# Performance work log

Hardware: AMD Instinct MI355X
Metric: run time of the kernel (lower is better)

Reference implementation:

```python
import jax, jax.numpy as jnp
import numpy as np

B, N_MM, N_V, N_A = 2, 256, 64, 128
DIM, HEADS, ATTN_RATIO, MLP_RATIO = 1024, 16, 0.25, 4.0
INNER = int(DIM * ATTN_RATIO)          # 256
HID = int(DIM * MLP_RATIO)             # 4096
SCALE = (DIM // HEADS) ** -0.5         # faithful to source: uses dim//num_heads
EPS = 1e-5


def setup_inputs() -> dict:
    key = jax.random.key(0)
    ks = jax.random.split(key, 16)
    s = 0.02
    return {
        "xmm": jax.random.normal(ks[0], (B, N_MM, DIM), jnp.float32),
        "xv": jax.random.normal(ks[1], (B, N_V, DIM), jnp.float32),
        "xa": jax.random.normal(ks[2], (B, N_A, DIM), jnp.float32),
        "ln_mm_w": jnp.ones((DIM,), jnp.float32),
        "ln_mm_b": jnp.zeros((DIM,), jnp.float32),
        "ln_v_w": jnp.ones((DIM,), jnp.float32),
        "ln_v_b": jnp.zeros((DIM,), jnp.float32),
        "ln_a_w": jnp.ones((DIM,), jnp.float32),
        "ln_a_b": jnp.zeros((DIM,), jnp.float32),
        "Wq": jax.random.normal(ks[3], (DIM, INNER), jnp.float32) * s,
        "Wkv": jax.random.normal(ks[4], (2 * DIM, 2 * INNER), jnp.float32) * s,
        "Wproj": jax.random.normal(ks[5], (INNER, DIM), jnp.float32) * s,
        "bproj": jnp.zeros((DIM,), jnp.float32),
        "ln_mlp_w": jnp.ones((DIM,), jnp.float32),
        "ln_mlp_b": jnp.zeros((DIM,), jnp.float32),
        "W1": jax.random.normal(ks[6], (DIM, HID), jnp.float32) * s,
        "b1": jnp.zeros((HID,), jnp.float32),
        "W2": jax.random.normal(ks[7], (HID, DIM), jnp.float32) * s,
        "b2": jnp.zeros((DIM,), jnp.float32),
    }


def _ln(x, w, b):
    m = x.mean(-1, keepdims=True)
    v = ((x - m) ** 2).mean(-1, keepdims=True)
    return (x - m) / jnp.sqrt(v + EPS) * w + b


def reference(xmm, xv, xa, ln_mm_w, ln_mm_b, ln_v_w, ln_v_b, ln_a_w, ln_a_b,
              Wq, Wkv, Wproj, bproj, ln_mlp_w, ln_mlp_b, W1, b1, W2, b2):
    hd = INNER // HEADS
    src_mm = _ln(xmm, ln_mm_w, ln_mm_b)
    src_v = _ln(xv, ln_v_w, ln_v_b)
    src_a = _ln(xa, ln_a_w, ln_a_b)

    # kv(x_va) where x_va = cat([xv broadcast over N_a, xa broadcast over N_v], -1).
    # Equivalent to projecting each stream separately and broadcast-adding:
    kv_v = src_v @ Wkv[:DIM]            # [B, N_v, 2*INNER]
    kv_a = src_a @ Wkv[DIM:]            # [B, N_a, 2*INNER]
    kv = kv_v[:, :, None, :] + kv_a[:, None, :, :]          # [B, N_v, N_a, 2*INNER]
    kv = kv.reshape(B, N_V * N_A, 2, HEADS, hd)
    k = kv[:, :, 0].transpose(0, 2, 1, 3)                   # [B, H, N_va, hd]
    v = kv[:, :, 1].transpose(0, 2, 1, 3)

    q = (src_mm @ Wq).reshape(B, N_MM, HEADS, hd).transpose(0, 2, 1, 3)

    attn = jnp.einsum('bhqd,bhkd->bhqk', q, k) * SCALE
    attn = jax.nn.softmax(attn, axis=-1)
    out = jnp.einsum('bhqk,bhkd->bhqd', attn, v)
    out = out.transpose(0, 2, 1, 3).reshape(B, N_MM, INNER)
    out = out @ Wproj + bproj

    xmm = xmm + out
    h = _ln(xmm, ln_mlp_w, ln_mlp_b)
    h = jax.nn.gelu(h @ W1 + b1, approximate=False) @ W2 + b2
    return xmm + h
```

## Files before the change

### kernel.cpp

```cpp
#include <hip/hip_runtime.h>
#include <hip/hip_bf16.h>
#include <math.h>


typedef unsigned short ushort_t;
typedef __attribute__((ext_vector_type(8))) __bf16 bf16x8;
typedef __attribute__((ext_vector_type(4))) float f32x4;

#define DEVFN static __device__ __forceinline__

DEVFN float bf2f(ushort_t u) {
    return __uint_as_float(((unsigned int)u) << 16);
}
DEVFN ushort_t f2bf(float f) {
    unsigned int x = __float_as_uint(f);
    unsigned int r = x + 0x7FFFu + ((x >> 16) & 1u);
    return (ushort_t)(r >> 16);
}
DEVFN void unpack8(uint4 dv, float* dst) {
    unsigned int ws[4] = {dv.x, dv.y, dv.z, dv.w};
#pragma unroll
    for (int i = 0; i < 4; i++) {
        dst[2 * i] = __uint_as_float(ws[i] << 16);
        dst[2 * i + 1] = __uint_as_float(ws[i] & 0xFFFF0000u);
    }
}

DEVFN void ln_body(const float* __restrict__ x, const float* __restrict__ w,
                   const float* __restrict__ b, ushort_t* __restrict__ out,
                   int row) {
    const float4* xr4 = (const float4*)(x + (size_t)row * 1024);
    ushort_t* orow = out + (size_t)row * 1024;
    int tid = threadIdx.x;
    float4 v4 = xr4[tid];
    float s = v4.x + v4.y + v4.z + v4.w;
    float ss = v4.x * v4.x + v4.y * v4.y + v4.z * v4.z + v4.w * v4.w;
#pragma unroll
    for (int off = 32; off > 0; off >>= 1) {
        s += __shfl_down(s, off);
        ss += __shfl_down(ss, off);
    }
    __shared__ float red[8];
    if ((tid & 63) == 0) {
        red[tid >> 6] = s;
        red[4 + (tid >> 6)] = ss;
    }
    __syncthreads();
    s = red[0] + red[1] + red[2] + red[3];
    ss = red[4] + red[5] + red[6] + red[7];
    float mean = s * (1.f / 1024.f);
    float var = ss * (1.f / 1024.f) - mean * mean;
    float rstd = rsqrtf(var + 1e-5f);
    const float4 w4 = ((const float4*)w)[tid];
    const float4 b4 = ((const float4*)b)[tid];
    union { ushort_t u[4]; uint2 v; } pk;
    pk.u[0] = f2bf((v4.x - mean) * rstd * w4.x + b4.x);
    pk.u[1] = f2bf((v4.y - mean) * rstd * w4.y + b4.y);
    pk.u[2] = f2bf((v4.z - mean) * rstd * w4.z + b4.z);
    pk.u[3] = f2bf((v4.w - mean) * rstd * w4.w + b4.w);
    *(uint2*)(&orow[tid * 4]) = pk.v;
}

__global__ __launch_bounds__(256) void ln_kernel(
    const float* __restrict__ x, const float* __restrict__ w,
    const float* __restrict__ b, ushort_t* __restrict__ out) {
    ln_body(x, w, b, out, blockIdx.x);
}

struct LNSeg {
    const float* x; const float* w; const float* b; ushort_t* out; int start;
};
struct TDesc { const float* in; ushort_t* out; int R, C, nx, start; };

__global__ __launch_bounds__(256) void prep_kernel(LNSeg l0, LNSeg l1,
                                                   LNSeg l2, TDesc d0,
                                                   TDesc d1, TDesc d2,
                                                   TDesc d3, TDesc d4) {
    int id = blockIdx.x;
    if (id < 896) {
        LNSeg s = (id >= l2.start) ? l2 : ((id >= l1.start) ? l1 : l0);
        ln_body(s.x, s.w, s.b, s.out, id - s.start);
        return;
    }
    id -= 896;
    TDesc d = (id >= d4.start) ? d4
            : (id >= d3.start) ? d3
            : (id >= d2.start) ? d2
            : (id >= d1.start) ? d1 : d0;
    int t = id - d.start;
    int bx = (t % d.nx) * 32;
    int by = (t / d.nx) * 32;
    __shared__ ushort_t tile[32][33];
    int tx = threadIdx.x & 31;
    int ty = threadIdx.x >> 5;
    for (int i = ty; i < 32; i += 8)
        tile[i][tx] = f2bf(d.in[(size_t)(by + i) * d.C + bx + tx]);
    __syncthreads();
    for (int i = ty; i < 32; i += 8)
        d.out[(size_t)(bx + i) * d.R + by + tx] = tile[tx][i];
}

template <int EPI, typename OutT>
DEVFN void gemm64_core(const ushort_t* __restrict__ A, int lda,
                       const ushort_t* __restrict__ B, int ldb,
                       OutT* __restrict__ C, int ldc,
                       const float* __restrict__ bias,
                       const float* __restrict__ resid, int K, int m0, int n0,
                       ushort_t* As, ushort_t* Bs) {
    constexpr int LS = 40;
    int tid = threadIdx.x;
    int wave = tid >> 6, lane = tid & 63;
    int wm = wave >> 1, wn = wave & 1;
    int quad = lane >> 4, l16 = lane & 15;

    f32x4 acc[2][2];
#pragma unroll
    for (int i = 0; i < 2; i++)
#pragma unroll
        for (int j = 0; j < 2; j++) acc[i][j] = (f32x4){0.f, 0.f, 0.f, 0.f};

    int r = tid >> 2, c = tid & 3;
    const ushort_t* Ap = A + (size_t)(m0 + r) * lda + c * 8;
    const ushort_t* Bp = B + (size_t)(n0 + r) * ldb + c * 8;
    uint4 ra = *(const uint4*)Ap;
    uint4 rb = *(const uint4*)Bp;

    for (int k0 = 0; k0 < K; k0 += 32) {
        *(uint4*)(&As[r * LS + c * 8]) = ra;
        *(uint4*)(&Bs[r * LS + c * 8]) = rb;
        __syncthreads();
        if (k0 + 32 < K) {
            ra = *(const uint4*)(Ap + k0 + 32);
            rb = *(const uint4*)(Bp + k0 + 32);
        }
        bf16x8 af[2], bfr[2];
#pragma unroll
        for (int i = 0; i < 2; i++)
            af[i] = *(const bf16x8*)(&As[(wm * 32 + i * 16 + l16) * LS + quad * 8]);
#pragma unroll
        for (int j = 0; j < 2; j++)
            bfr[j] = *(const bf16x8*)(&Bs[(wn * 32 + j * 16 + l16) * LS + quad * 8]);
#pragma unroll
        for (int i = 0; i < 2; i++)
#pragma unroll
            for (int j = 0; j < 2; j++)
                acc[i][j] = __builtin_amdgcn_mfma_f32_16x16x32_bf16(
                    af[i], bfr[j], acc[i][j], 0, 0, 0);
        __syncthreads();
    }

#pragma unroll
    for (int i = 0; i < 2; i++)
#pragma unroll
        for (int j = 0; j < 2; j++) {
            int col = n0 + wn * 32 + j * 16 + l16;
            int rbase = m0 + wm * 32 + i * 16 + quad * 4;
            float bv = (EPI == 2 || EPI == 3) ? bias[col] : 0.f;
#pragma unroll
            for (int rr = 0; rr < 4; rr++) {
                int row = rbase + rr;
                float vv = acc[i][j][rr] + bv;
                if (EPI == 2) vv = 0.5f * vv * (1.f + erff(vv * 0.70710678118654752f));
                if (EPI == 3) vv += resid[(size_t)row * ldc + col];
                if constexpr (sizeof(OutT) == 2)
                    C[(size_t)row * ldc + col] = (OutT)f2bf(vv);
                else
                    C[(size_t)row * ldc + col] = vv;
            }
        }
}

template <int EPI, typename OutT>
__global__ __launch_bounds__(256) void gemm64(
    const ushort_t* __restrict__ A, int lda, const ushort_t* __restrict__ Bt,
    int ldb, OutT* __restrict__ C, int ldc, const float* __restrict__ bias,
    const float* __restrict__ resid, int Kper, int sliceStride) {
    __shared__ ushort_t As[64 * 40];
    __shared__ ushort_t Bs[64 * 40];
    int z = blockIdx.z;
    gemm64_core<EPI, OutT>(A + (size_t)z * Kper, lda, Bt + (size_t)z * Kper,
                           ldb, C + (size_t)z * sliceStride, ldc, bias, resid,
                           Kper, blockIdx.y * 64, blockIdx.x * 64, As, Bs);
}

struct GSeg {
    const ushort_t* A; const ushort_t* B; ushort_t* C;
    int lda, ldb, ldc, nx, start;
};
__global__ __launch_bounds__(256) void gemm64_multi(GSeg s0, GSeg s1, GSeg s2,
                                                    int K) {
    __shared__ ushort_t As[64 * 40];
    __shared__ ushort_t Bs[64 * 40];
    int id = blockIdx.x;
    GSeg s = (id >= s2.start) ? s2 : ((id >= s1.start) ? s1 : s0);
    int t = id - s.start;
    int n0 = (t % s.nx) * 64;
    int m0 = (t / s.nx) * 64;
    gemm64_core<0, ushort_t>(s.A, s.lda, s.B, s.ldb, s.C, s.ldc, nullptr,
                             nullptr, K, m0, n0, As, Bs);
}

__global__ __launch_bounds__(256) void reduce_mlp2(
    const float* __restrict__ P, const float* __restrict__ y,
    const float* __restrict__ b2, float* __restrict__ out) {
    int i = blockIdx.x * 256 + threadIdx.x;
    const float4* p = (const float4*)P;
    float4 a = p[i], b = p[i + 131072], cc = p[i + 2 * 131072],
           d = p[i + 3 * 131072];
    float4 yy = ((const float4*)y)[i];
    float4 bb = ((const float4*)b2)[i & 255];
    float4 o;
    o.x = a.x + b.x + cc.x + d.x + yy.x + bb.x;
    o.y = a.y + b.y + cc.y + d.y + yy.y + bb.y;
    o.z = a.z + b.z + cc.z + d.z + yy.z + bb.z;
    o.w = a.w + b.w + cc.w + d.w + yy.w + bb.w;
    ((float4*)out)[i] = o;
}

__global__ __launch_bounds__(256) void attn_kernel(
    const ushort_t* __restrict__ q, const ushort_t* __restrict__ kvv,
    const ushort_t* __restrict__ kva, ushort_t* __restrict__ out) {
    int bh = blockIdx.x;
    int b = bh >> 4, h = bh & 15;
    int tid = threadIdx.x;

    __shared__ float Kv[64][16], Vv[64][16], Ka[128][16], Va[128][16];

    {
        int row = tid >> 2, seg = (tid >> 1) & 1, half = tid & 1;
        const ushort_t* src =
            kvv + (size_t)(b * 64 + row) * 512 + seg * 256 + h * 16 + half * 8;
        float* dst = (seg ? Vv[row] : Kv[row]) + half * 8;
        unpack8(*(const uint4*)src, dst);
    }
#pragma unroll
    for (int t2 = 0; t2 < 2; t2++) {
        int t = tid + t2 * 256;
        int row = t >> 2, seg = (t >> 1) & 1, half = t & 1;
        const ushort_t* src =
            kva + (size_t)(b * 128 + row) * 512 + seg * 256 + h * 16 + half * 8;
        float* dst = (seg ? Va[row] : Ka[row]) + half * 8;
        unpack8(*(const uint4*)src, dst);
    }
    __syncthreads();

    int qlocal = tid >> 2;
    int dg = tid & 3;
    int qrow = blockIdx.y * 64 + qlocal;
    const ushort_t* qp = q + (size_t)(b * 256 + qrow) * 256 + h * 16 + dg * 4;
    uint2 qu = *(const uint2*)qp;
    float4 qv;
    qv.x = __uint_as_float(qu.x << 16) * 0.125f;
    qv.y = __uint_as_float(qu.x & 0xFFFF0000u) * 0.125f;
    qv.z = __uint_as_float(qu.y << 16) * 0.125f;
    qv.w = __uint_as_float(qu.y & 0xFFFF0000u) * 0.125f;

    const float4* Kv4 = (const float4*)Kv;
    const float4* Vv4 = (const float4*)Vv;
    const float4* Ka4 = (const float4*)Ka;
    const float4* Va4 = (const float4*)Va;

    float4 ov = {0.f, 0.f, 0.f, 0.f};
    float den = 0.f;
#pragma unroll 8
    for (int i = 0; i < 64; i++) {
        float4 kk = Kv4[i * 4 + dg];
        float part = qv.x * kk.x + qv.y * kk.y + qv.z * kk.z + qv.w * kk.w;
        part += __shfl_xor(part, 1);
        part += __shfl_xor(part, 2);
        float p = __expf(part);
        den += p;
        float4 vv = Vv4[i * 4 + dg];
        ov.x += p * vv.x; ov.y += p * vv.y; ov.z += p * vv.z; ov.w += p * vv.w;
    }
    float4 oa = {0.f, 0.f, 0.f, 0.f};
    float dena = 0.f;
#pragma unroll 8
    for (int i = 0; i < 128; i++) {
        float4 kk = Ka4[i * 4 + dg];
        float part = qv.x * kk.x + qv.y * kk.y + qv.z * kk.z + qv.w * kk.w;
        part += __shfl_xor(part, 1);
        part += __shfl_xor(part, 2);
        float p = __expf(part);
        dena += p;
        float4 vv = Va4[i * 4 + dg];
        oa.x += p * vv.x; oa.y += p * vv.y; oa.z += p * vv.z; oa.w += p * vv.w;
    }

    float rv = 1.f / den, ra = 1.f / dena;
    union { ushort_t u[4]; uint2 v; } pk;
    pk.u[0] = f2bf(ov.x * rv + oa.x * ra);
    pk.u[1] = f2bf(ov.y * rv + oa.y * ra);
    pk.u[2] = f2bf(ov.z * rv + oa.z * ra);
    pk.u[3] = f2bf(ov.w * rv + oa.w * ra);
    *(uint2*)(out + (size_t)(b * 256 + qrow) * 256 + h * 16 + dg * 4) = pk.v;
}

extern "C" void kernel_launch(void* const* d_in, const int* in_sizes, int n_in,
                              void* d_out, int out_size, void* d_ws,
                              size_t ws_size, hipStream_t stream) {
    const float* xmm = (const float*)d_in[0];
    const float* xv = (const float*)d_in[1];
    const float* xa = (const float*)d_in[2];
    const float* ln_mm_w = (const float*)d_in[3];
    const float* ln_mm_b = (const float*)d_in[4];
    const float* ln_v_w = (const float*)d_in[5];
    const float* ln_v_b = (const float*)d_in[6];
    const float* ln_a_w = (const float*)d_in[7];
    const float* ln_a_b = (const float*)d_in[8];
    const float* Wq = (const float*)d_in[9];
    const float* Wkv = (const float*)d_in[10];
    const float* Wproj = (const float*)d_in[11];
    const float* bproj = (const float*)d_in[12];
    const float* ln_mlp_w = (const float*)d_in[13];
    const float* ln_mlp_b = (const float*)d_in[14];
    const float* W1 = (const float*)d_in[15];
    const float* b1 = (const float*)d_in[16];
    const float* W2 = (const float*)d_in[17];
    const float* b2 = (const float*)d_in[18];
    float* outp = (float*)d_out;

    char* w = (char*)d_ws;
    ushort_t* xmmN = (ushort_t*)w;    w += 512 * 1024 * 2;
    ushort_t* xvN = (ushort_t*)w;     w += 128 * 1024 * 2;
    ushort_t* xaN = (ushort_t*)w;     w += 256 * 1024 * 2;
    ushort_t* Wqt = (ushort_t*)w;     w += 256 * 1024 * 2;
    ushort_t* Wkvt = (ushort_t*)w;    w += 512 * 2048 * 2;
    ushort_t* Wprojt = (ushort_t*)w;  w += 1024 * 256 * 2;
    ushort_t* W1t = (ushort_t*)w;     w += 4096 * 1024 * 2;
    ushort_t* W2t = (ushort_t*)w;     w += 1024 * 4096 * 2;
    ushort_t* qout = (ushort_t*)w;    w += 512 * 256 * 2;
    ushort_t* kvvb = (ushort_t*)w;    w += 128 * 512 * 2;
    ushort_t* kvab = (ushort_t*)w;    w += 256 * 512 * 2;
    ushort_t* attnout = (ushort_t*)w; w += 512 * 256 * 2;
    float* y = (float*)w;             w += 512 * 1024 * 4;
    ushort_t* h0 = (ushort_t*)w;      w += 512 * 1024 * 2;
    ushort_t* g = (ushort_t*)w;       w += 512 * 4096 * 2;
    float* P = (float*)w;             w += 4 * 512 * 1024 * 4;

    LNSeg L0{xmm, ln_mm_w, ln_mm_b, xmmN, 0};
    LNSeg L1{xv, ln_v_w, ln_v_b, xvN, 512};
    LNSeg L2{xa, ln_a_w, ln_a_b, xaN, 640};
    TDesc T0{Wq, Wqt, 1024, 256, 8, 0};
    TDesc T1{Wkv, Wkvt, 2048, 512, 16, 256};
    TDesc T2{Wproj, Wprojt, 256, 1024, 32, 1280};
    TDesc T3{W1, W1t, 1024, 4096, 128, 1536};
    TDesc T4{W2, W2t, 4096, 1024, 32, 5632};
    prep_kernel<<<896 + 9728, 256, 0, stream>>>(L0, L1, L2, T0, T1, T2, T3, T4);

    GSeg G0{xmmN, Wqt, qout, 1024, 1024, 256, 4, 0};
    GSeg G1{xvN, Wkvt, kvvb, 1024, 2048, 512, 8, 32};
    GSeg G2{xaN, Wkvt + 1024, kvab, 1024, 2048, 512, 8, 48};
    gemm64_multi<<<80, 256, 0, stream>>>(G0, G1, G2, 1024);

    attn_kernel<<<dim3(32, 4), 256, 0, stream>>>(qout, kvvb, kvab, attnout);

    gemm64<3, float><<<dim3(16, 8, 1), 256, 0, stream>>>(
        attnout, 256, Wprojt, 256, y, 1024, bproj, xmm, 256, 0);

    ln_kernel<<<512, 256, 0, stream>>>(y, ln_mlp_w, ln_mlp_b, h0);

    gemm64<2, ushort_t><<<dim3(64, 8, 1), 256, 0, stream>>>(
        h0, 1024, W1t, 1024, g, 4096, b1, nullptr, 1024, 0);

    gemm64<4, float><<<dim3(16, 8, 4), 256, 0, stream>>>(
        g, 4096, W2t, 4096, P, 1024, nullptr, nullptr, 1024, 512 * 1024);

    reduce_mlp2<<<512, 256, 0, stream>>>(P, y, b2, outp);

    (void)in_sizes; (void)n_in; (void)out_size; (void)ws_size;
}
```

Measured before the change: 201.9 us.

## Fuse all stages into one cooperative persistent kernel with grid syncs

Replaces the eight separate kernel launches with a single cooperative mega-kernel of 512 persistent blocks. Each stage loops over its work items and is separated from the next by grid.sync(). The aim is to remove per-launch overhead and the inter-kernel gaps. The weight-transpose tiles are also changed to use float4 loads and packed uint2 stores. The cost is that every stage boundary becomes a grid-wide barrier, and small stages (80 or 128 items) leave most of the 512 blocks idle.

```diff
diff --git a/kernel.cpp b/kernel.cpp
--- a/kernel.cpp
+++ b/kernel.cpp
@@ -1,6 +1,9 @@
 #include <hip/hip_runtime.h>
 #include <hip/hip_bf16.h>
+#include <hip/hip_cooperative_groups.h>
 #include <math.h>
+
+namespace cg = cooperative_groups;
 
 
 typedef unsigned short ushort_t;
@@ -26,9 +29,23 @@
     }
 }
 
+struct MegaParams {
+    const float *xmm, *xv, *xa;
+    const float *ln_mm_w, *ln_mm_b, *ln_v_w, *ln_v_b, *ln_a_w, *ln_a_b;
+    const float *Wq, *Wkv, *Wproj, *bproj, *ln_mlp_w, *ln_mlp_b;
+    const float *W1, *b1, *W2, *b2;
+    float* outp;
+    ushort_t *xmmN, *xvN, *xaN;
+    ushort_t *Wqt, *Wkvt, *Wprojt, *W1t, *W2t;
+    ushort_t *qout, *kvvb, *kvab, *attnout;
+    float* y;
+    ushort_t *h0, *g;
+    float* P;
+};
+
 DEVFN void ln_body(const float* __restrict__ x, const float* __restrict__ w,
                    const float* __restrict__ b, ushort_t* __restrict__ out,
-                   int row) {
+                   int row, float* red) {
     const float4* xr4 = (const float4*)(x + (size_t)row * 1024);
     ushort_t* orow = out + (size_t)row * 1024;
     int tid = threadIdx.x;
@@ -40,7 +57,6 @@
         s += __shfl_down(s, off);
         ss += __shfl_down(ss, off);
     }
-    __shared__ float red[8];
     if ((tid & 63) == 0) {
         red[tid >> 6] = s;
         red[4 + (tid >> 6)] = ss;
@@ -61,52 +77,13 @@
     *(uint2*)(&orow[tid * 4]) = pk.v;
 }
 
-__global__ __launch_bounds__(256) void ln_kernel(
-    const float* __restrict__ x, const float* __restrict__ w,
-    const float* __restrict__ b, ushort_t* __restrict__ out) {
-    ln_body(x, w, b, out, blockIdx.x);
-}
-
-struct LNSeg {
-    const float* x; const float* w; const float* b; ushort_t* out; int start;
-};
-struct TDesc { const float* in; ushort_t* out; int R, C, nx, start; };
-
-__global__ __launch_bounds__(256) void prep_kernel(LNSeg l0, LNSeg l1,
-                                                   LNSeg l2, TDesc d0,
-                                                   TDesc d1, TDesc d2,
-                                                   TDesc d3, TDesc d4) {
-    int id = blockIdx.x;
-    if (id < 896) {
-        LNSeg s = (id >= l2.start) ? l2 : ((id >= l1.start) ? l1 : l0);
-        ln_body(s.x, s.w, s.b, s.out, id - s.start);
-        return;
-    }
-    id -= 896;
-    TDesc d = (id >= d4.start) ? d4
-            : (id >= d3.start) ? d3
-            : (id >= d2.start) ? d2
-            : (id >= d1.start) ? d1 : d0;
-    int t = id - d.start;
-    int bx = (t % d.nx) * 32;
-    int by = (t / d.nx) * 32;
-    __shared__ ushort_t tile[32][33];
-    int tx = threadIdx.x & 31;
-    int ty = threadIdx.x >> 5;
-    for (int i = ty; i < 32; i += 8)
-        tile[i][tx] = f2bf(d.in[(size_t)(by + i) * d.C + bx + tx]);
-    __syncthreads();
-    for (int i = ty; i < 32; i += 8)
-        d.out[(size_t)(bx + i) * d.R + by + tx] = tile[tx][i];
-}
-
 template <int EPI, typename OutT>
-DEVFN void gemm64_core(const ushort_t* __restrict__ A, int lda,
-                       const ushort_t* __restrict__ B, int ldb,
-                       OutT* __restrict__ C, int ldc,
-                       const float* __restrict__ bias,
-                       const float* __restrict__ resid, int K, int m0, int n0,
-                       ushort_t* As, ushort_t* Bs) {
+DEVFN void gemm_item(const ushort_t* __restrict__ A, int lda,
+                     const ushort_t* __restrict__ B, int ldb,
+                     OutT* __restrict__ C, int ldc,
+                     const float* __restrict__ bias,
+                     const float* __restrict__ resid, int K, int m0, int n0,
+                     ushort_t* As, ushort_t* Bs) {
     constexpr int LS = 40;
     int tid = threadIdx.x;
     int wave = tid >> 6, lane = tid & 63;
@@ -170,203 +147,256 @@
         }
 }
 
-template <int EPI, typename OutT>
-__global__ __launch_bounds__(256) void gemm64(
-    const ushort_t* __restrict__ A, int lda, const ushort_t* __restrict__ Bt,
-    int ldb, OutT* __restrict__ C, int ldc, const float* __restrict__ bias,
-    const float* __restrict__ resid, int Kper, int sliceStride) {
-    __shared__ ushort_t As[64 * 40];
-    __shared__ ushort_t Bs[64 * 40];
-    int z = blockIdx.z;
-    gemm64_core<EPI, OutT>(A + (size_t)z * Kper, lda, Bt + (size_t)z * Kper,
-                           ldb, C + (size_t)z * sliceStride, ldc, bias, resid,
-                           Kper, blockIdx.y * 64, blockIdx.x * 64, As, Bs);
-}
-
-struct GSeg {
-    const ushort_t* A; const ushort_t* B; ushort_t* C;
-    int lda, ldb, ldc, nx, start;
-};
-__global__ __launch_bounds__(256) void gemm64_multi(GSeg s0, GSeg s1, GSeg s2,
-                                                    int K) {
-    __shared__ ushort_t As[64 * 40];
-    __shared__ ushort_t Bs[64 * 40];
-    int id = blockIdx.x;
-    GSeg s = (id >= s2.start) ? s2 : ((id >= s1.start) ? s1 : s0);
-    int t = id - s.start;
-    int n0 = (t % s.nx) * 64;
-    int m0 = (t / s.nx) * 64;
-    gemm64_core<0, ushort_t>(s.A, s.lda, s.B, s.ldb, s.C, s.ldc, nullptr,
-                             nullptr, K, m0, n0, As, Bs);
-}
-
-__global__ __launch_bounds__(256) void reduce_mlp2(
-    const float* __restrict__ P, const float* __restrict__ y,
-    const float* __restrict__ b2, float* __restrict__ out) {
-    int i = blockIdx.x * 256 + threadIdx.x;
-    const float4* p = (const float4*)P;
-    float4 a = p[i], b = p[i + 131072], cc = p[i + 2 * 131072],
-           d = p[i + 3 * 131072];
-    float4 yy = ((const float4*)y)[i];
-    float4 bb = ((const float4*)b2)[i & 255];
-    float4 o;
-    o.x = a.x + b.x + cc.x + d.x + yy.x + bb.x;
-    o.y = a.y + b.y + cc.y + d.y + yy.y + bb.y;
-    o.z = a.z + b.z + cc.z + d.z + yy.z + bb.z;
-    o.w = a.w + b.w + cc.w + d.w + yy.w + bb.w;
-    ((float4*)out)[i] = o;
-}
-
-__global__ __launch_bounds__(256) void attn_kernel(
-    const ushort_t* __restrict__ q, const ushort_t* __restrict__ kvv,
-    const ushort_t* __restrict__ kva, ushort_t* __restrict__ out) {
-    int bh = blockIdx.x;
-    int b = bh >> 4, h = bh & 15;
+__global__ __launch_bounds__(256, 2) void mega_kernel(MegaParams p) {
+    cg::grid_group grid = cg::this_grid();
+    __shared__ alignas(16) unsigned char smem[24576];
     int tid = threadIdx.x;
-
-    __shared__ float Kv[64][16], Vv[64][16], Ka[128][16], Va[128][16];
-
-    {
-        int row = tid >> 2, seg = (tid >> 1) & 1, half = tid & 1;
-        const ushort_t* src =
-            kvv + (size_t)(b * 64 + row) * 512 + seg * 256 + h * 16 + half * 8;
-        float* dst = (seg ? Vv[row] : Kv[row]) + half * 8;
-        unpack8(*(const uint4*)src, dst);
-    }
-#pragma unroll
-    for (int t2 = 0; t2 < 2; t2++) {
-        int t = tid + t2 * 256;
-        int row = t >> 2, seg = (t >> 1) & 1, half = t & 1;
-        const ushort_t* src =
-            kva + (size_t)(b * 128 + row) * 512 + seg * 256 + h * 16 + half * 8;
-        float* dst = (seg ? Va[row] : Ka[row]) + half * 8;
-        unpack8(*(const uint4*)src, dst);
-    }
-    __syncthreads();
-
-    int qlocal = tid >> 2;
-    int dg = tid & 3;
-    int qrow = blockIdx.y * 64 + qlocal;
-    const ushort_t* qp = q + (size_t)(b * 256 + qrow) * 256 + h * 16 + dg * 4;
-    uint2 qu = *(const uint2*)qp;
-    float4 qv;
-    qv.x = __uint_as_float(qu.x << 16) * 0.125f;
-    qv.y = __uint_as_float(qu.x & 0xFFFF0000u) * 0.125f;
-    qv.z = __uint_as_float(qu.y << 16) * 0.125f;
-    qv.w = __uint_as_float(qu.y & 0xFFFF0000u) * 0.125f;
-
-    const float4* Kv4 = (const float4*)Kv;
-    const float4* Vv4 = (const float4*)Vv;
-    const float4* Ka4 = (const float4*)Ka;
-    const float4* Va4 = (const float4*)Va;
-
-    float4 ov = {0.f, 0.f, 0.f, 0.f};
-    float den = 0.f;
+    int nb = gridDim.x;
+
+    {
+        float* red = (float*)smem;
+        ushort_t* tile = (ushort_t*)smem;
+        for (int t = blockIdx.x; t < 896 + 9728; t += nb) {
+            if (t < 896) {
+                const float *x, *w, *b; ushort_t* o; int start;
+                if (t >= 640)      { x = p.xa;  w = p.ln_a_w;  b = p.ln_a_b;  o = p.xaN;  start = 640; }
+                else if (t >= 512) { x = p.xv;  w = p.ln_v_w;  b = p.ln_v_b;  o = p.xvN;  start = 512; }
+                else               { x = p.xmm; w = p.ln_mm_w; b = p.ln_mm_b; o = p.xmmN; start = 0; }
+                ln_body(x, w, b, o, t - start, red);
+            } else {
+                int id = t - 896;
+                const float* in; ushort_t* out; int R, C, nx, start;
+                if (id >= 5632)      { in = p.W2;    out = p.W2t;    R = 4096; C = 1024; nx = 32;  start = 5632; }
+                else if (id >= 1536) { in = p.W1;    out = p.W1t;    R = 1024; C = 4096; nx = 128; start = 1536; }
+                else if (id >= 1280) { in = p.Wproj; out = p.Wprojt; R = 256;  C = 1024; nx = 32;  start = 1280; }
+                else if (id >= 256)  { in = p.Wkv;   out = p.Wkvt;   R = 2048; C = 512;  nx = 16;  start = 256; }
+                else                 { in = p.Wq;    out = p.Wqt;    R = 1024; C = 256;  nx = 8;   start = 0; }
+                int tt = id - start;
+                int bx = (tt % nx) * 32;
+                int by = (tt / nx) * 32;
+                int r = tid >> 3, c4 = (tid & 7) * 4;
+                float4 f = *(const float4*)(in + (size_t)(by + r) * C + bx + c4);
+                ushort_t* tr = tile + r * 33 + c4;
+                tr[0] = f2bf(f.x); tr[1] = f2bf(f.y);
+                tr[2] = f2bf(f.z); tr[3] = f2bf(f.w);
+                __syncthreads();
+                int oc = tid >> 3, or4 = (tid & 7) * 4;
+                union { ushort_t u[4]; uint2 v; } pk;
+#pragma unroll
+                for (int j = 0; j < 4; j++) pk.u[j] = tile[(or4 + j) * 33 + oc];
+                *(uint2*)(out + (size_t)(bx + oc) * R + by + or4) = pk.v;
+            }
+            __syncthreads();
+        }
+    }
+    grid.sync();
+
+    {
+        ushort_t* As = (ushort_t*)smem;
+        ushort_t* Bs = As + 64 * 40;
+        for (int t = blockIdx.x; t < 80; t += nb) {
+            const ushort_t *A, *B; ushort_t* C; int lda, ldb, ldc, nx, start;
+            if (t >= 48)      { A = p.xaN;  B = p.Wkvt + 1024; C = p.kvab; lda = 1024; ldb = 2048; ldc = 512; nx = 8; start = 48; }
+            else if (t >= 32) { A = p.xvN;  B = p.Wkvt;        C = p.kvvb; lda = 1024; ldb = 2048; ldc = 512; nx = 8; start = 32; }
+            else              { A = p.xmmN; B = p.Wqt;         C = p.qout; lda = 1024; ldb = 1024; ldc = 256; nx = 4; start = 0; }
+            int tt = t - start;
+            gemm_item<0, ushort_t>(A, lda, B, ldb, C, ldc, nullptr, nullptr,
+                                   1024, (tt / nx) * 64, (tt % nx) * 64, As, Bs);
+        }
+    }
+    grid.sync();
+
+    {
+        float* Kv = (float*)smem;
+        float* Vv = Kv + 64 * 16;
+        float* Ka = Vv + 64 * 16;
+        float* Va = Ka + 128 * 16;
+        for (int t = blockIdx.x; t < 128; t += nb) {
+            int bh = t & 31, qc = t >> 5;
+            int b = bh >> 4, h = bh & 15;
+            {
+                int row = tid >> 2, seg = (tid >> 1) & 1, half = tid & 1;
+                const ushort_t* src = p.kvvb + (size_t)(b * 64 + row) * 512 +
+                                      seg * 256 + h * 16 + half * 8;
+                float* dst = (seg ? Vv : Kv) + row * 16 + half * 8;
+                unpack8(*(const uint4*)src, dst);
+            }
+#pragma unroll
+            for (int t2 = 0; t2 < 2; t2++) {
+                int tt = tid + t2 * 256;
+                int row = tt >> 2, seg = (tt >> 1) & 1, half = tt & 1;
+                const ushort_t* src = p.kvab + (size_t)(b * 128 + row) * 512 +
+                                      seg * 256 + h * 16 + half * 8;
+                float* dst = (seg ? Va : Ka) + row * 16 + half * 8;
+                unpack8(*(const uint4*)src, dst);
+            }
+            __syncthreads();
+
+            int qlocal = tid >> 2;
+            int dg = tid & 3;
+            int qrow = qc * 64 + qlocal;
+            const ushort_t* qp =
+                p.qout + (size_t)(b * 256 + qrow) * 256 + h * 16 + dg * 4;
+            uint2 qu = *(const uint2*)qp;
+            float4 qv;
+            qv.x = __uint_as_float(qu.x << 16) * 0.125f;
+            qv.y = __uint_as_float(qu.x & 0xFFFF0000u) * 0.125f;
+            qv.z = __uint_as_float(qu.y << 16) * 0.125f;
+            qv.w = __uint_as_float(qu.y & 0xFFFF0000u) * 0.125f;
+
+            const float4* Kv4 = (const float4*)Kv;
+            const float4* Vv4 = (const float4*)Vv;
+            const float4* Ka4 = (const float4*)Ka;
+            const float4* Va4 = (const float4*)Va;
+
+            float4 ov = {0.f, 0.f, 0.f, 0.f};
+            float den = 0.f;
 #pragma unroll 8
-    for (int i = 0; i < 64; i++) {
-        float4 kk = Kv4[i * 4 + dg];
-        float part = qv.x * kk.x + qv.y * kk.y + qv.z * kk.z + qv.w * kk.w;
-        part += __shfl_xor(part, 1);
-        part += __shfl_xor(part, 2);
-        float p = __expf(part);
-        den += p;
-        float4 vv = Vv4[i * 4 + dg];
-        ov.x += p * vv.x; ov.y += p * vv.y; ov.z += p * vv.z; ov.w += p * vv.w;
-    }
-    float4 oa = {0.f, 0.f, 0.f, 0.f};
-    float dena = 0.f;
+            for (int i = 0; i < 64; i++) {
+                float4 kk = Kv4[i * 4 + dg];
+                float part = qv.x * kk.x + qv.y * kk.y + qv.z * kk.z + qv.w * kk.w;
+                part += __shfl_xor(part, 1);
+                part += __shfl_xor(part, 2);
+                float pe = __expf(part);
+                den += pe;
+                float4 vv = Vv4[i * 4 + dg];
+                ov.x += pe * vv.x; ov.y += pe * vv.y;
+                ov.z += pe * vv.z; ov.w += pe * vv.w;
+            }
+            float4 oa = {0.f, 0.f, 0.f, 0.f};
+            float dena = 0.f;
 #pragma unroll 8
-    for (int i = 0; i < 128; i++) {
-        float4 kk = Ka4[i * 4 + dg];
-        float part = qv.x * kk.x + qv.y * kk.y + qv.z * kk.z + qv.w * kk.w;
-        part += __shfl_xor(part, 1);
-        part += __shfl_xor(part, 2);
-        float p = __expf(part);
-        dena += p;
-        float4 vv = Va4[i * 4 + dg];
-        oa.x += p * vv.x; oa.y += p * vv.y; oa.z += p * vv.z; oa.w += p * vv.w;
-    }
-
-    float rv = 1.f / den, ra = 1.f / dena;
-    union { ushort_t u[4]; uint2 v; } pk;
-    pk.u[0] = f2bf(ov.x * rv + oa.x * ra);
-    pk.u[1] = f2bf(ov.y * rv + oa.y * ra);
-    pk.u[2] = f2bf(ov.z * rv + oa.z * ra);
-    pk.u[3] = f2bf(ov.w * rv + oa.w * ra);
-    *(uint2*)(out + (size_t)(b * 256 + qrow) * 256 + h * 16 + dg * 4) = pk.v;
+            for (int i = 0; i < 128; i++) {
+                float4 kk = Ka4[i * 4 + dg];
+                float part = qv.x * kk.x + qv.y * kk.y + qv.z * kk.z + qv.w * kk.w;
+                part += __shfl_xor(part, 1);
+                part += __shfl_xor(part, 2);
+                float pe = __expf(part);
+                dena += pe;
+                float4 vv = Va4[i * 4 + dg];
+                oa.x += pe * vv.x; oa.y += pe * vv.y;
+                oa.z += pe * vv.z; oa.w += pe * vv.w;
+            }
+
+            float rv = 1.f / den, ra = 1.f / dena;
+            union { ushort_t u[4]; uint2 v; } pk;
+            pk.u[0] = f2bf(ov.x * rv + oa.x * ra);
+            pk.u[1] = f2bf(ov.y * rv + oa.y * ra);
+            pk.u[2] = f2bf(ov.z * rv + oa.z * ra);
+            pk.u[3] = f2bf(ov.w * rv + oa.w * ra);
+            *(uint2*)(p.attnout + (size_t)(b * 256 + qrow) * 256 + h * 16 +
+                      dg * 4) = pk.v;
+            __syncthreads();
+        }
+    }
+    grid.sync();
+
+    {
+        ushort_t* As = (ushort_t*)smem;
+        ushort_t* Bs = As + 64 * 40;
+        for (int t = blockIdx.x; t < 128; t += nb)
+            gemm_item<3, float>(p.attnout, 256, p.Wprojt, 256, p.y, 1024,
+                                p.bproj, p.xmm, 256, (t >> 4) * 64,
+                                (t & 15) * 64, As, Bs);
+    }
+    grid.sync();
+
+    {
+        float* red = (float*)smem;
+        for (int t = blockIdx.x; t < 512; t += nb) {
+            ln_body(p.y, p.ln_mlp_w, p.ln_mlp_b, p.h0, t, red);
+            __syncthreads();
+        }
+    }
+    grid.sync();
+
+    {
+        ushort_t* As = (ushort_t*)smem;
+        ushort_t* Bs = As + 64 * 40;
+        for (int t = blockIdx.x; t < 512; t += nb)
+            gemm_item<2, ushort_t>(p.h0, 1024, p.W1t, 1024, p.g, 4096, p.b1,
+                                   nullptr, 1024, (t >> 6) * 64, (t & 63) * 64,
+                                   As, Bs);
+    }
+    grid.sync();
+
+    {
+        ushort_t* As = (ushort_t*)smem;
+        ushort_t* Bs = As + 64 * 40;
+        for (int t = blockIdx.x; t < 512; t += nb) {
+            int z = t >> 7, rem = t & 127;
+            gemm_item<4, float>(p.g + z * 1024, 4096, p.W2t + z * 1024, 4096,
+                                p.P + (size_t)z * 512 * 1024, 1024, nullptr,
+                                nullptr, 1024, (rem >> 4) * 64, (rem & 15) * 64,
+                                As, Bs);
+        }
+    }
+    grid.sync();
+
+    {
+        for (int t = blockIdx.x; t < 512; t += nb) {
+            int i = t * 256 + tid;
+            const float4* pp = (const float4*)p.P;
+            float4 a = pp[i], b = pp[i + 131072], cc = pp[i + 2 * 131072],
+                   d = pp[i + 3 * 131072];
+            float4 yy = ((const float4*)p.y)[i];
+            float4 bb = ((const float4*)p.b2)[i & 255];
+            float4 o;
+            o.x = a.x + b.x + cc.x + d.x + yy.x + bb.x;
+            o.y = a.y + b.y + cc.y + d.y + yy.y + bb.y;
+            o.z = a.z + b.z + cc.z + d.z + yy.z + bb.z;
+            o.w = a.w + b.w + cc.w + d.w + yy.w + bb.w;
+            ((float4*)p.outp)[i] = o;
+        }
+    }
 }
 
 extern "C" void kernel_launch(void* const* d_in, const int* in_sizes, int n_in,
                               void* d_out, int out_size, void* d_ws,
                               size_t ws_size, hipStream_t stream) {
-    const float* xmm = (const float*)d_in[0];
-    const float* xv = (const float*)d_in[1];
-    const float* xa = (const float*)d_in[2];
-    const float* ln_mm_w = (const float*)d_in[3];
-    const float* ln_mm_b = (const float*)d_in[4];
-    const float* ln_v_w = (const float*)d_in[5];
-    const float* ln_v_b = (const float*)d_in[6];
-    const float* ln_a_w = (const float*)d_in[7];
-    const float* ln_a_b = (const float*)d_in[8];
-    const float* Wq = (const float*)d_in[9];
-    const float* Wkv = (const float*)d_in[10];
-    const float* Wproj = (const float*)d_in[11];
-    const float* bproj = (const float*)d_in[12];
-    const float* ln_mlp_w = (const float*)d_in[13];
-    const float* ln_mlp_b = (const float*)d_in[14];
-    const float* W1 = (const float*)d_in[15];
-    const float* b1 = (const float*)d_in[16];
-    const float* W2 = (const float*)d_in[17];
-    const float* b2 = (const float*)d_in[18];
-    float* outp = (float*)d_out;
+    MegaParams p;
+    p.xmm = (const float*)d_in[0];
+    p.xv = (const float*)d_in[1];
+    p.xa = (const float*)d_in[2];
+    p.ln_mm_w = (const float*)d_in[3];
+    p.ln_mm_b = (const float*)d_in[4];
+    p.ln_v_w = (const float*)d_in[5];
+    p.ln_v_b = (const float*)d_in[6];
+    p.ln_a_w = (const float*)d_in[7];
+    p.ln_a_b = (const float*)d_in[8];
+    p.Wq = (const float*)d_in[9];
+    p.Wkv = (const float*)d_in[10];
+    p.Wproj = (const float*)d_in[11];
+    p.bproj = (const float*)d_in[12];
+    p.ln_mlp_w = (const float*)d_in[13];
+    p.ln_mlp_b = (const float*)d_in[14];
+    p.W1 = (const float*)d_in[15];
+    p.b1 = (const float*)d_in[16];
+    p.W2 = (const float*)d_in[17];
+    p.b2 = (const float*)d_in[18];
+    p.outp = (float*)d_out;
 
     char* w = (char*)d_ws;
-    ushort_t* xmmN = (ushort_t*)w;    w += 512 * 1024 * 2;
-    ushort_t* xvN = (ushort_t*)w;     w += 128 * 1024 * 2;
-    ushort_t* xaN = (ushort_t*)w;     w += 256 * 1024 * 2;
-    ushort_t* Wqt = (ushort_t*)w;     w += 256 * 1024 * 2;
-    ushort_t* Wkvt = (ushort_t*)w;    w += 512 * 2048 * 2;
-    ushort_t* Wprojt = (ushort_t*)w;  w += 1024 * 256 * 2;
-    ushort_t* W1t = (ushort_t*)w;     w += 4096 * 1024 * 2;
-    ushort_t* W2t = (ushort_t*)w;     w += 1024 * 4096 * 2;
-    ushort_t* qout = (ushort_t*)w;    w += 512 * 256 * 2;
-    ushort_t* kvvb = (ushort_t*)w;    w += 128 * 512 * 2;
-    ushort_t* kvab = (ushort_t*)w;    w += 256 * 512 * 2;
-    ushort_t* attnout = (ushort_t*)w; w += 512 * 256 * 2;
-    float* y = (float*)w;             w += 512 * 1024 * 4;
-    ushort_t* h0 = (ushort_t*)w;      w += 512 * 1024 * 2;
-    ushort_t* g = (ushort_t*)w;       w += 512 * 4096 * 2;
-    float* P = (float*)w;             w += 4 * 512 * 1024 * 4;
-
-    LNSeg L0{xmm, ln_mm_w, ln_mm_b, xmmN, 0};
-    LNSeg L1{xv, ln_v_w, ln_v_b, xvN, 512};
-    LNSeg L2{xa, ln_a_w, ln_a_b, xaN, 640};
-    TDesc T0{Wq, Wqt, 1024, 256, 8, 0};
-    TDesc T1{Wkv, Wkvt, 2048, 512, 16, 256};
-    TDesc T2{Wproj, Wprojt, 256, 1024, 32, 1280};
-    TDesc T3{W1, W1t, 1024, 4096, 128, 1536};
-    TDesc T4{W2, W2t, 4096, 1024, 32, 5632};
-    prep_kernel<<<896 + 9728, 256, 0, stream>>>(L0, L1, L2, T0, T1, T2, T3, T4);
-
-    GSeg G0{xmmN, Wqt, qout, 1024, 1024, 256, 4, 0};
-    GSeg G1{xvN, Wkvt, kvvb, 1024, 2048, 512, 8, 32};
-    GSeg G2{xaN, Wkvt + 1024, kvab, 1024, 2048, 512, 8, 48};
-    gemm64_multi<<<80, 256, 0, stream>>>(G0, G1, G2, 1024);
-
-    attn_kernel<<<dim3(32, 4), 256, 0, stream>>>(qout, kvvb, kvab, attnout);
-
-    gemm64<3, float><<<dim3(16, 8, 1), 256, 0, stream>>>(
-        attnout, 256, Wprojt, 256, y, 1024, bproj, xmm, 256, 0);
-
-    ln_kernel<<<512, 256, 0, stream>>>(y, ln_mlp_w, ln_mlp_b, h0);
-
-    gemm64<2, ushort_t><<<dim3(64, 8, 1), 256, 0, stream>>>(
-        h0, 1024, W1t, 1024, g, 4096, b1, nullptr, 1024, 0);
-
-    gemm64<4, float><<<dim3(16, 8, 4), 256, 0, stream>>>(
-        g, 4096, W2t, 4096, P, 1024, nullptr, nullptr, 1024, 512 * 1024);
-
-    reduce_mlp2<<<512, 256, 0, stream>>>(P, y, b2, outp);
+    p.xmmN = (ushort_t*)w;    w += 512 * 1024 * 2;
+    p.xvN = (ushort_t*)w;     w += 128 * 1024 * 2;
+    p.xaN = (ushort_t*)w;     w += 256 * 1024 * 2;
+    p.Wqt = (ushort_t*)w;     w += 256 * 1024 * 2;
+    p.Wkvt = (ushort_t*)w;    w += 512 * 2048 * 2;
+    p.Wprojt = (ushort_t*)w;  w += 1024 * 256 * 2;
+    p.W1t = (ushort_t*)w;     w += 4096 * 1024 * 2;
+    p.W2t = (ushort_t*)w;     w += 1024 * 4096 * 2;
+    p.qout = (ushort_t*)w;    w += 512 * 256 * 2;
+    p.kvvb = (ushort_t*)w;    w += 128 * 512 * 2;
+    p.kvab = (ushort_t*)w;    w += 256 * 512 * 2;
+    p.attnout = (ushort_t*)w; w += 512 * 256 * 2;
+    p.y = (float*)w;          w += 512 * 1024 * 4;
+    p.h0 = (ushort_t*)w;      w += 512 * 1024 * 2;
+    p.g = (ushort_t*)w;       w += 512 * 4096 * 2;
+    p.P = (float*)w;          w += 4 * 512 * 1024 * 4;
+
+    void* kargs[] = {(void*)&p};
+    hipLaunchCooperativeKernel((void*)mega_kernel, dim3(512), dim3(256), kargs,
+                               0, stream);
 
     (void)in_sizes; (void)n_in; (void)out_size; (void)ws_size;
 }
```

New measurement: 622.3 us. 208% more time.
